# Kernel tuning notes

Hardware: AMD Instinct MI355X
Metric: run time of the kernel (lower is better)

## Reference

```python
import jax, jax.numpy as jnp
import numpy as np

B, S, D = 4, 2048, 1024


def setup_inputs() -> dict:
    key = jax.random.key(0)
    ks = jax.random.split(key, 9)
    scale = 1.0 / np.sqrt(D)
    x = jax.random.normal(ks[0], (B, S, D), dtype=jnp.float32)
    mask = jnp.tril(jnp.ones((S, S), dtype=jnp.int32))[None, :, :]  # causal, broadcast over batch
    Wq = jax.random.normal(ks[1], (D, D), dtype=jnp.float32) * scale
    bq = jax.random.normal(ks[2], (D,), dtype=jnp.float32) * 0.01
    Wk = jax.random.normal(ks[3], (D, D), dtype=jnp.float32) * scale
    bk = jax.random.normal(ks[4], (D,), dtype=jnp.float32) * 0.01
    Wv = jax.random.normal(ks[5], (D, D), dtype=jnp.float32) * scale
    bv = jax.random.normal(ks[6], (D,), dtype=jnp.float32) * 0.01
    Wo = jax.random.normal(ks[7], (D, D), dtype=jnp.float32) * scale
    bo = jax.random.normal(ks[8], (D,), dtype=jnp.float32) * 0.01
    return {"x": x, "mask": mask, "Wq": Wq, "bq": bq, "Wk": Wk, "bk": bk,
            "Wv": Wv, "bv": bv, "Wo": Wo, "bo": bo}


def reference(x, mask, Wq, bq, Wk, bk, Wv, bv, Wo, bo):
    # Linear projections (torch Linear: x @ W^T + b; here W stored as [in, out])
    Q = jnp.einsum('bsd,de->bse', x, Wq) + bq
    K = jnp.einsum('bsd,de->bse', x, Wk) + bk
    V = jnp.einsum('bsd,de->bse', x, Wv) + bv
    d_k = Q.shape[-1]
    scores = jnp.einsum('bqd,bkd->bqk', Q, K) / jnp.sqrt(jnp.float32(d_k))
    scores = jnp.where(mask == 0, jnp.float32(-jnp.inf), scores)
    attn_weights = jax.nn.softmax(scores, axis=-1)  # [B, S, S]
    attn_output = jnp.einsum('bqk,bkd->bqd', attn_weights, V)
    output = jnp.einsum('bsd,de->bse', attn_output, Wo) + bo
    return output, attn_weights
```

## Files before the change

kernel.cpp:

```cpp
#include <hip/hip_runtime.h>
#include <cstdint>
#include <cstddef>
#include <cmath>

typedef __bf16 bf16_t;
typedef bf16_t bf16x8 __attribute__((ext_vector_type(8)));
typedef bf16_t bf16x4 __attribute__((ext_vector_type(4)));
typedef float f32x4 __attribute__((ext_vector_type(4)));

constexpr int kB = 4;
constexpr int kS = 2048;
constexpr int kD = 1024;
constexpr int BM = 128, BN = 128, BK = 32;
constexpr int TILE_ELEMS = (BM + BN) * BK;

typedef __attribute__((address_space(1))) void as1void;
typedef __attribute__((address_space(3))) void as3void;

__device__ __forceinline__ void gload16(const void* g, void* l) {
  __builtin_amdgcn_global_load_lds((as1void*)g, (as3void*)l, 16, 0, 0);
}

__device__ __forceinline__ void wgbar() {
  asm volatile("" ::: "memory");
  __builtin_amdgcn_s_barrier();
  asm volatile("" ::: "memory");
}

__device__ __forceinline__ void gemm_mainloop(
    const bf16_t* __restrict__ A, int lda,
    const bf16_t* __restrict__ B, int ldb,
    int ksteps, bf16_t* lds, f32x4 acc[4][4]) {
  const int tid = threadIdx.x;
  const int w = tid >> 6, lane = tid & 63;
  const int srow = lane >> 2;
  const int scol = (lane & 3) << 3;
  const int wr = (w >> 1) << 6, wc = (w & 1) << 6;
  const int fr = lane & 15, kg = lane >> 4;

  const bf16_t* ga0 = A + (size_t)(w * 16 + srow) * lda + scol;
  const bf16_t* ga1 = A + (size_t)(64 + w * 16 + srow) * lda + scol;
  const bf16_t* gb0 = B + (size_t)(w * 16 + srow) * ldb + scol;
  const bf16_t* gb1 = B + (size_t)(64 + w * 16 + srow) * ldb + scol;
  const int oa0 = (w * 16) * BK;
  const int oa1 = (64 + w * 16) * BK;
  const int ob0 = BM * BK + (w * 16) * BK;
  const int ob1 = BM * BK + (64 + w * 16) * BK;

  gload16(ga0, lds + oa0);
  gload16(ga1, lds + oa1);
  gload16(gb0, lds + ob0);
  gload16(gb1, lds + ob1);
  ga0 += BK; ga1 += BK; gb0 += BK; gb1 += BK;
  __syncthreads();

  int cur = 0;
  for (int ks = 0; ks < ksteps; ++ks) {
    const int nxt = cur ^ 1;
    if (ks + 1 < ksteps) {
      bf16_t* nb = lds + nxt * TILE_ELEMS;
      gload16(ga0, nb + oa0);
      gload16(ga1, nb + oa1);
      gload16(gb0, nb + ob0);
      gload16(gb1, nb + ob1);
      ga0 += BK; ga1 += BK; gb0 += BK; gb1 += BK;
    }
    const bf16_t* cb = lds + cur * TILE_ELEMS;
    bf16x8 af[4], bfv[4];
#pragma unroll
    for (int m = 0; m < 4; ++m)
      af[m] = *(const bf16x8*)(cb + (wr + m * 16 + fr) * BK + kg * 8);
#pragma unroll
    for (int n = 0; n < 4; ++n)
      bfv[n] = *(const bf16x8*)(cb + BM * BK + (wc + n * 16 + fr) * BK + kg * 8);
#pragma unroll
    for (int m = 0; m < 4; ++m)
#pragma unroll
      for (int n = 0; n < 4; ++n)
        acc[m][n] = __builtin_amdgcn_mfma_f32_16x16x32_bf16(af[m], bfv[n],
                                                            acc[m][n], 0, 0, 0);
    __syncthreads();
    cur = nxt;
  }
}

__device__ __forceinline__ void gemm256_loop(
    const bf16_t* __restrict__ A, int lda,
    const bf16_t* __restrict__ B, int ldb,
    int nk, bf16_t* lds, f32x4 acc[8][4]) {
  const int tid = threadIdx.x;
  const int wid = tid >> 6, lane = tid & 63;
  const int wm = wid >> 2, wn = wid & 3;
  const int fr = lane & 15, kg = (lane >> 4) & 3;
  const int s_row = ((tid >> 7) << 4) | (tid & 15);
  const int s_col = ((tid >> 4) & 7) << 3;
  const bf16_t* pA = A + (size_t)s_row * lda + s_col;
  const bf16_t* pB = B + (size_t)s_row * ldb + s_col;
  const int ldst = wid << 9;

  auto stg = [&](int tt, int op, int h, int j) {
    const bf16_t* g = (op ? pB : pA) + (size_t)(h * 128 + j * 64) * (op ? ldb : lda)
                      + (size_t)tt * 64;
    bf16_t* d = lds + (((tt & 1) * 4 + op * 2 + h) * 8192) + j * 4096 + ldst;
    gload16(g, d);
  };

#pragma unroll
  for (int h = 0; h < 2; ++h)
#pragma unroll
    for (int j = 0; j < 2; ++j) { stg(0, 0, h, j); stg(0, 1, h, j); }
  stg(1, 1, 0, 0); stg(1, 1, 0, 1); stg(1, 1, 1, 0); stg(1, 1, 1, 1);
  stg(1, 0, 0, 0); stg(1, 0, 1, 0);
  asm volatile("s_waitcnt vmcnt(6)" ::: "memory");
  wgbar();

  const int arow = kg * 128 + fr * 8;
  for (int t = 0; t < nk; ++t) {
    const bf16_t* sb = lds + (t & 1) * 32768;
    const bf16_t* aslot = sb + wm * 8192;
    const bf16_t* bslot = sb + (2 + (wn >> 1)) * 8192 + (wn & 1) * 4096;
    bf16x8 bF[4][2];
#pragma unroll
    for (int q = 0; q < 4; ++q) {
      bf16x8 aF[2][2];
#pragma unroll
      for (int mi = 0; mi < 2; ++mi)
#pragma unroll
        for (int ks = 0; ks < 2; ++ks)
          aF[mi][ks] = *(const bf16x8*)(aslot + (2 * q + mi) * 1024 + ks * 512 + arow);
      if (q == 0) {
#pragma unroll
        for (int n = 0; n < 4; ++n)
#pragma unroll
          for (int ks = 0; ks < 2; ++ks)
            bF[n][ks] = *(const bf16x8*)(bslot + n * 1024 + ks * 512 + arow);
      }
      if (q == 0)      { if (t + 1 <= nk - 1) { stg(t + 1, 0, 0, 1); stg(t + 1, 0, 1, 1); } }
      else if (q == 1) { if (t + 2 <= nk - 1) { stg(t + 2, 1, 0, 0); stg(t + 2, 1, 0, 1); } }
      else if (q == 2) { if (t + 2 <= nk - 1) { stg(t + 2, 1, 1, 0); stg(t + 2, 1, 1, 1); } }
      else             { if (t + 2 <= nk - 1) { stg(t + 2, 0, 0, 0); stg(t + 2, 0, 1, 0); } }
      wgbar();
      __builtin_amdgcn_s_setprio(1);
#pragma unroll
      for (int mi = 0; mi < 2; ++mi)
#pragma unroll
        for (int n = 0; n < 4; ++n)
#pragma unroll
          for (int ks = 0; ks < 2; ++ks)
            acc[2 * q + mi][n] = __builtin_amdgcn_mfma_f32_16x16x32_bf16(
                aF[mi][ks], bF[n][ks], acc[2 * q + mi][n], 0, 0, 0);
      __builtin_amdgcn_s_setprio(0);
      asm volatile("s_waitcnt lgkmcnt(0)" ::: "memory");
      if (q == 3 && t < nk - 1) {
        if (t + 2 <= nk - 1) asm volatile("s_waitcnt vmcnt(6)" ::: "memory");
        else                 asm volatile("s_waitcnt vmcnt(0)" ::: "memory");
      }
      wgbar();
    }
  }
}


__global__ __launch_bounds__(512, 2)
void k_qk256(const bf16_t* __restrict__ A, const bf16_t* __restrict__ WT,
             const float* __restrict__ bq, const float* __restrict__ bk,
             bf16_t* __restrict__ Qb, bf16_t* __restrict__ Kb) {
  __shared__ bf16_t lds[65536];
  const int id = blockIdx.x;
  const int swz = (id & 7) * 32 + (id >> 3);
  const int mb = swz >> 3, nb = swz & 7;
  const int m0 = mb * 256, n0 = nb * 256;
  f32x4 acc[8][4] = {};
  gemm256_loop(A + (size_t)m0 * kD, kD, WT + (size_t)n0 * kD, kD,
               kD / 64, lds, acc);
  const int lane = threadIdx.x & 63, wid = threadIdx.x >> 6;
  const int wm = wid >> 2, wn = wid & 3, fr = lane & 15, kgr = lane >> 4;
  const int which = n0 >> 10;
  bf16_t* C = which == 0 ? Qb : Kb;
  const float* bias = which == 0 ? bq : bk;
#pragma unroll
  for (int n = 0; n < 4; ++n) {
    const int col = (n0 & 1023) + wn * 64 + n * 16 + fr;
    const float bvv = bias[col];
#pragma unroll
    for (int m = 0; m < 8; ++m)
#pragma unroll
      for (int i = 0; i < 4; ++i) {
        const int row = m0 + wm * 128 + m * 16 + kgr * 4 + i;
        C[(size_t)row * kD + col] = (bf16_t)(acc[m][n][i] + bvv);
      }
  }
}

__global__ __launch_bounds__(256)
void k_scores_v(const bf16_t* __restrict__ Q, const bf16_t* __restrict__ K,
                float* __restrict__ Sc,
                const bf16_t* __restrict__ X, const bf16_t* __restrict__ WvT,
                const float* __restrict__ bv, bf16_t* __restrict__ VT) {
  __shared__ bf16_t lds[2 * TILE_ELEMS];
  const int id = blockIdx.x;
  const int tid = threadIdx.x, w = tid >> 6, lane = tid & 63;
  const int wr = (w >> 1) << 6, wc = (w & 1) << 6, fr = lane & 15, kg = lane >> 4;
  if (id < 544) {
    const int b = id / 136, t = id % 136;
    int by = (int)((sqrtf(8.f * t + 1.f) - 1.f) * 0.5f);
    while ((by + 1) * (by + 2) / 2 <= t) ++by;
    while (by * (by + 1) / 2 > t) --by;
    const int bx = t - by * (by + 1) / 2;
    const int m0 = by * BM, n0 = bx * BN;
    f32x4 acc[4][4] = {};
    gemm_mainloop(Q + (size_t)b * kS * kD + (size_t)m0 * kD, kD,
                  K + (size_t)b * kS * kD + (size_t)n0 * kD, kD, kD / BK, lds, acc);
    float* Sb = Sc + (size_t)b * kS * kS;
#pragma unroll
    for (int m = 0; m < 4; ++m)
#pragma unroll
      for (int n = 0; n < 4; ++n)
#pragma unroll
        for (int i = 0; i < 4; ++i) {
          const int row = m0 + wr + m * 16 + kg * 4 + i;
          const int col = n0 + wc + n * 16 + fr;
          Sb[(size_t)row * kS + col] = acc[m][n][i] * 0.03125f;
        }
  } else {
    const int vid = id - 544;
    const int swz = (vid & 7) * 64 + (vid >> 3);
    const int m0 = (swz >> 3) * BM, n0 = (swz & 7) * BN;
    f32x4 acc[4][4] = {};
    gemm_mainloop(X + (size_t)m0 * kD, kD, WvT + (size_t)n0 * kD, kD,
                  kD / BK, lds, acc);
#pragma unroll
    for (int n = 0; n < 4; ++n) {
      const int col = n0 + wc + n * 16 + fr;
      const float bvv = bv[col];
#pragma unroll
      for (int m = 0; m < 4; ++m)
#pragma unroll
        for (int i = 0; i < 4; ++i) {
          const int row = m0 + wr + m * 16 + kg * 4 + i;
          const int b = row >> 11, s = row & (kS - 1);
          VT[((size_t)b * kD + col) * kS + s] = (bf16_t)(acc[m][n][i] + bvv);
        }
    }
  }
}

__global__ __launch_bounds__(256)
void k_softmax(float* __restrict__ P, bf16_t* __restrict__ Pb) {
  const int row = blockIdx.x;
  const int q = row & (kS - 1);
  float* p = P + (size_t)row * kS;
  bf16_t* pb = Pb + (size_t)row * kS;
  const int L = q + 1;
  __shared__ float buf[kS];
  __shared__ float red[8];
  const int tid = threadIdx.x;
  float4* b4 = (float4*)buf;
  const float4* p4 = (const float4*)p;
  if (tid * 4 < L) b4[tid] = p4[tid];
  if (1024 + tid * 4 < L) b4[tid + 256] = p4[tid + 256];
  __syncthreads();
  float mx = -1e30f;
  for (int k = tid; k < L; k += 256) mx = fmaxf(mx, buf[k]);
#pragma unroll
  for (int s2 = 32; s2 >= 1; s2 >>= 1) mx = fmaxf(mx, __shfl_xor(mx, s2));
  if ((tid & 63) == 0) red[tid >> 6] = mx;
  __syncthreads();
  mx = fmaxf(fmaxf(red[0], red[1]), fmaxf(red[2], red[3]));
  float sm = 0.f;
  for (int k = tid; k < L; k += 256) {
    const float e = __expf(buf[k] - mx);
    buf[k] = e;
    sm += e;
  }
#pragma unroll
  for (int s2 = 32; s2 >= 1; s2 >>= 1) sm += __shfl_xor(sm, s2);
  if ((tid & 63) == 0) red[4 + (tid >> 6)] = sm;
  __syncthreads();
  const float inv = 1.f / (red[4] + red[5] + red[6] + red[7]);
  for (int k = tid; k < L; k += 256) {
    const float v = buf[k] * inv;
    p[k] = v;
    pb[k] = (bf16_t)v;
  }
  for (int k = L + tid; k < kS; k += 256) p[k] = 0.f;
  const int bandEnd = (q & ~127) + 128;
  for (int k = L + tid; k < bandEnd; k += 256) pb[k] = (bf16_t)0.f;
}

__global__ __launch_bounds__(256)
void k_gemm_pv(const bf16_t* __restrict__ P, const bf16_t* __restrict__ VT,
               bf16_t* __restrict__ AO) {
  const int bx = blockIdx.x, b = blockIdx.z;
  const int by = (int)gridDim.y - 1 - (int)blockIdx.y;
  __shared__ bf16_t lds[2 * TILE_ELEMS];
  const int m0 = by * BM, n0 = bx * BN;
  const int ksteps = (m0 + BM) / BK;
  f32x4 acc[4][4] = {};
  gemm_mainloop(P + (size_t)b * kS * kS + (size_t)m0 * kS, kS,
                VT + (size_t)b * kD * kS + (size_t)n0 * kS, kS, ksteps, lds, acc);
  bf16_t* AOb = AO + (size_t)b * kS * kD;
  const int tid = threadIdx.x, w = tid >> 6, lane = tid & 63;
  const int wr = (w >> 1) << 6, wc = (w & 1) << 6, fr = lane & 15, kg = lane >> 4;
#pragma unroll
  for (int m = 0; m < 4; ++m)
#pragma unroll
    for (int n = 0; n < 4; ++n)
#pragma unroll
      for (int i = 0; i < 4; ++i) {
        const int row = m0 + wr + m * 16 + kg * 4 + i;
        const int col = n0 + wc + n * 16 + fr;
        AOb[(size_t)row * kD + col] = (bf16_t)acc[m][n][i];
      }
}

__global__ __launch_bounds__(256)
void k_gemm_out(const bf16_t* __restrict__ A, const bf16_t* __restrict__ Bw,
                const float* __restrict__ bias, float* __restrict__ C) {
  __shared__ bf16_t lds[2 * TILE_ELEMS];
  const int id = blockIdx.x;
  const int swz = (id & 7) * 64 + (id >> 3);
  const int m0 = (swz >> 3) * BM, n0 = (swz & 7) * BN;
  f32x4 acc[4][4] = {};
  gemm_mainloop(A + (size_t)m0 * kD, kD, Bw + (size_t)n0 * kD, kD, kD / BK, lds, acc);
  const int tid = threadIdx.x, w = tid >> 6, lane = tid & 63;
  const int wr = (w >> 1) << 6, wc = (w & 1) << 6, fr = lane & 15, kg = lane >> 4;
#pragma unroll
  for (int n = 0; n < 4; ++n) {
    const int col = n0 + wc + n * 16 + fr;
    const float bv = bias[col];
#pragma unroll
    for (int m = 0; m < 4; ++m)
#pragma unroll
      for (int i = 0; i < 4; ++i) {
        const int row = m0 + wr + m * 16 + kg * 4 + i;
        C[(size_t)row * kD + col] = acc[m][n][i] + bv;
      }
  }
}

__global__ __launch_bounds__(256)
void k_prep(const float* __restrict__ X, bf16_t* __restrict__ Y,
            const float* __restrict__ W0, const float* __restrict__ W1,
            const float* __restrict__ W2, const float* __restrict__ W3,
            bf16_t* __restrict__ T0, bf16_t* __restrict__ T1,
            bf16_t* __restrict__ T2, bf16_t* __restrict__ T3) {
  const int tx = threadIdx.x & 31, ty = threadIdx.x >> 5;
  if (blockIdx.z == 4) {
    const size_t n4 = (size_t)kB * kS * kD / 4;
    size_t i = ((size_t)blockIdx.y * 32 + blockIdx.x) * 256 + threadIdx.x;
    const size_t stride = (size_t)1024 * 256;
    const float4* X4 = (const float4*)X;
    bf16x4* Y4 = (bf16x4*)Y;
    for (; i < n4; i += stride) {
      const float4 v = X4[i];
      bf16x4 o = {(bf16_t)v.x, (bf16_t)v.y, (bf16_t)v.z, (bf16_t)v.w};
      Y4[i] = o;
    }
    return;
  }
  const float* W = blockIdx.z == 0 ? W0 : blockIdx.z == 1 ? W1 : blockIdx.z == 2 ? W2 : W3;
  bf16_t* T = blockIdx.z == 0 ? T0 : blockIdx.z == 1 ? T1 : blockIdx.z == 2 ? T2 : T3;
  __shared__ float t[32][33];
  const int x0 = blockIdx.x * 32, y0 = blockIdx.y * 32;
#pragma unroll
  for (int j = 0; j < 4; ++j)
    t[ty + 8 * j][tx] = W[(size_t)(y0 + ty + 8 * j) * kD + x0 + tx];
  __syncthreads();
#pragma unroll
  for (int j = 0; j < 4; ++j)
    T[(size_t)(x0 + ty + 8 * j) * kD + y0 + tx] = (bf16_t)t[tx][ty + 8 * j];
}

extern "C" void kernel_launch(void* const* d_in, const int* in_sizes, int n_in,
                              void* d_out, int out_size, void* d_ws, size_t ws_size,
                              hipStream_t stream) {
  (void)in_sizes; (void)n_in; (void)out_size; (void)ws_size;
  const float* x  = (const float*)d_in[0];
  const float* Wq = (const float*)d_in[2];
  const float* bq = (const float*)d_in[3];
  const float* Wk = (const float*)d_in[4];
  const float* bk = (const float*)d_in[5];
  const float* Wv = (const float*)d_in[6];
  const float* bv = (const float*)d_in[7];
  const float* Wo = (const float*)d_in[8];
  const float* bo = (const float*)d_in[9];

  float* out  = (float*)d_out;
  float* Pout = out + (size_t)kB * kS * kD;

  bf16_t* WqT = (bf16_t*)d_ws;
  bf16_t* WkT = WqT + (size_t)kD * kD;
  bf16_t* WvT = WkT + (size_t)kD * kD;
  bf16_t* WoT = WvT + (size_t)kD * kD;
  bf16_t* Qb  = WoT + (size_t)kD * kD;
  bf16_t* Kb  = Qb + (size_t)kB * kS * kD;
  bf16_t* VTb = Kb + (size_t)kB * kS * kD;
  bf16_t* Pb  = VTb + (size_t)kB * kS * kD;
  bf16_t* AOb = Pb + (size_t)kB * kS * kS;
  bf16_t* xb  = AOb + (size_t)kB * kS * kD;

  k_prep<<<dim3(32, 32, 5), 256, 0, stream>>>(x, xb, Wq, Wk, Wv, Wo,
                                              WqT, WkT, WvT, WoT);
  k_qk256<<<256, 512, 0, stream>>>(xb, WqT, bq, bk, Qb, Kb);
  k_scores_v<<<1056, 256, 0, stream>>>(Qb, Kb, Pout, xb, WvT, bv, VTb);
  k_softmax<<<kB * kS, 256, 0, stream>>>(Pout, Pb);
  k_gemm_pv<<<dim3(8, 16, kB), 256, 0, stream>>>(Pb, VTb, AOb);
  k_gemm_out<<<512, 256, 0, stream>>>(AOb, WoT, bo, out);
}
```

Measured before the change: 209.6 us.

## Move upper-triangle zeroing into scores kernel and register-resident softmax

The scores+V kernel gains 480 extra blocks that write zeros to the strictly upper-triangular 128x128 tiles of the fp32 attention-weight output. Block ids are interleaved so zeroing, QK^T and V-projection work mix across the grid. The softmax kernel keeps each row in registers as two float4 chunks instead of staging it through shared memory, and writes only up to the end of the diagonal band instead of zero-filling the whole row tail. The intent is to spread the large zero-fill writes across a GEMM-bound kernel and shorten the memory-bound softmax, at the cost of a larger grid and index remapping.

```diff
diff --git a/kernel.cpp b/kernel.cpp
--- a/kernel.cpp
+++ b/kernel.cpp
@@ -199,10 +199,11 @@
                 const float* __restrict__ bv, bf16_t* __restrict__ VT) {
   __shared__ bf16_t lds[2 * TILE_ELEMS];
   const int id = blockIdx.x;
+  const int wid0 = (id & 7) * 192 + (id >> 3);
   const int tid = threadIdx.x, w = tid >> 6, lane = tid & 63;
   const int wr = (w >> 1) << 6, wc = (w & 1) << 6, fr = lane & 15, kg = lane >> 4;
-  if (id < 544) {
-    const int b = id / 136, t = id % 136;
+  if (wid0 < 544) {
+    const int b = wid0 / 136, t = wid0 % 136;
     int by = (int)((sqrtf(8.f * t + 1.f) - 1.f) * 0.5f);
     while ((by + 1) * (by + 2) / 2 <= t) ++by;
     while (by * (by + 1) / 2 > t) --by;
@@ -222,10 +223,23 @@
           const int col = n0 + wc + n * 16 + fr;
           Sb[(size_t)row * kS + col] = acc[m][n][i] * 0.03125f;
         }
+  } else if (wid0 < 1024) {
+    const int zid = wid0 - 544;
+    const int b = zid / 120, u = zid % 120;
+    int r = (int)((1.f + sqrtf(8.f * u + 1.f)) * 0.5f);
+    while (r * (r - 1) / 2 > u) --r;
+    while ((r + 1) * r / 2 <= u) ++r;
+    const int c = u - r * (r - 1) / 2;
+    const int by = c, bx = r;
+    float* base = Sc + (size_t)b * kS * kS + (size_t)by * BM * kS + bx * BN;
+    const f32x4 z = {0.f, 0.f, 0.f, 0.f};
+    for (int i = tid; i < 128 * 32; i += 256) {
+      const int row = i >> 5, c4 = i & 31;
+      ((f32x4*)(base + (size_t)row * kS))[c4] = z;
+    }
   } else {
-    const int vid = id - 544;
-    const int swz = (vid & 7) * 64 + (vid >> 3);
-    const int m0 = (swz >> 3) * BM, n0 = (swz & 7) * BN;
+    const int vid = wid0 - 1024;
+    const int m0 = (vid >> 3) * BM, n0 = (vid & 7) * BN;
     f32x4 acc[4][4] = {};
     gemm_mainloop(X + (size_t)m0 * kD, kD, WvT + (size_t)n0 * kD, kD,
                   kD / BK, lds, acc);
@@ -249,43 +263,56 @@
 void k_softmax(float* __restrict__ P, bf16_t* __restrict__ Pb) {
   const int row = blockIdx.x;
   const int q = row & (kS - 1);
+  const int L = q + 1;
+  const int nch = (q >> 2) + 1;
+  const int nB = ((q & ~127) + 128) >> 2;
   float* p = P + (size_t)row * kS;
-  bf16_t* pb = Pb + (size_t)row * kS;
-  const int L = q + 1;
-  __shared__ float buf[kS];
+  f32x4* p4 = (f32x4*)p;
+  bf16x4* pb4 = (bf16x4*)(Pb + (size_t)row * kS);
+  const int tid = threadIdx.x;
+  const int c0 = tid, c1 = 256 + tid;
+  f32x4 v0 = {-1e30f, -1e30f, -1e30f, -1e30f}, v1 = v0;
+  if (c0 < nch) v0 = p4[c0];
+  if (c1 < nch) v1 = p4[c1];
+#pragma unroll
+  for (int j = 0; j < 4; ++j) {
+    if (4 * c0 + j >= L) v0[j] = -1e30f;
+    if (4 * c1 + j >= L) v1[j] = -1e30f;
+  }
+  float mx = -1e30f;
+#pragma unroll
+  for (int j = 0; j < 4; ++j) mx = fmaxf(mx, fmaxf(v0[j], v1[j]));
+#pragma unroll
+  for (int s2 = 32; s2 >= 1; s2 >>= 1) mx = fmaxf(mx, __shfl_xor(mx, s2));
   __shared__ float red[8];
-  const int tid = threadIdx.x;
-  float4* b4 = (float4*)buf;
-  const float4* p4 = (const float4*)p;
-  if (tid * 4 < L) b4[tid] = p4[tid];
-  if (1024 + tid * 4 < L) b4[tid + 256] = p4[tid + 256];
-  __syncthreads();
-  float mx = -1e30f;
-  for (int k = tid; k < L; k += 256) mx = fmaxf(mx, buf[k]);
-#pragma unroll
-  for (int s2 = 32; s2 >= 1; s2 >>= 1) mx = fmaxf(mx, __shfl_xor(mx, s2));
   if ((tid & 63) == 0) red[tid >> 6] = mx;
   __syncthreads();
   mx = fmaxf(fmaxf(red[0], red[1]), fmaxf(red[2], red[3]));
+  f32x4 e0, e1;
   float sm = 0.f;
-  for (int k = tid; k < L; k += 256) {
-    const float e = __expf(buf[k] - mx);
-    buf[k] = e;
-    sm += e;
+#pragma unroll
+  for (int j = 0; j < 4; ++j) {
+    e0[j] = (4 * c0 + j < L) ? __expf(v0[j] - mx) : 0.f;
+    e1[j] = (4 * c1 + j < L) ? __expf(v1[j] - mx) : 0.f;
+    sm += e0[j] + e1[j];
   }
 #pragma unroll
   for (int s2 = 32; s2 >= 1; s2 >>= 1) sm += __shfl_xor(sm, s2);
   if ((tid & 63) == 0) red[4 + (tid >> 6)] = sm;
   __syncthreads();
   const float inv = 1.f / (red[4] + red[5] + red[6] + red[7]);
-  for (int k = tid; k < L; k += 256) {
-    const float v = buf[k] * inv;
-    p[k] = v;
-    pb[k] = (bf16_t)v;
-  }
-  for (int k = L + tid; k < kS; k += 256) p[k] = 0.f;
-  const int bandEnd = (q & ~127) + 128;
-  for (int k = L + tid; k < bandEnd; k += 256) pb[k] = (bf16_t)0.f;
+  if (c0 < nB) {
+    f32x4 o; bf16x4 ob;
+#pragma unroll
+    for (int j = 0; j < 4; ++j) { o[j] = e0[j] * inv; ob[j] = (bf16_t)o[j]; }
+    p4[c0] = o; pb4[c0] = ob;
+  }
+  if (c1 < nB) {
+    f32x4 o; bf16x4 ob;
+#pragma unroll
+    for (int j = 0; j < 4; ++j) { o[j] = e1[j] * inv; ob[j] = (bf16_t)o[j]; }
+    p4[c1] = o; pb4[c1] = ob;
+  }
 }
 
 __global__ __launch_bounds__(256)
@@ -403,7 +430,7 @@
   k_prep<<<dim3(32, 32, 5), 256, 0, stream>>>(x, xb, Wq, Wk, Wv, Wo,
                                               WqT, WkT, WvT, WoT);
   k_qk256<<<256, 512, 0, stream>>>(xb, WqT, bq, bk, Qb, Kb);
-  k_scores_v<<<1056, 256, 0, stream>>>(Qb, Kb, Pout, xb, WvT, bv, VTb);
+  k_scores_v<<<1536, 256, 0, stream>>>(Qb, Kb, Pout, xb, WvT, bv, VTb);
   k_softmax<<<kB * kS, 256, 0, stream>>>(Pout, Pb);
   k_gemm_pv<<<dim3(8, 16, kB), 256, 0, stream>>>(Pb, VTb, AOb);
   k_gemm_out<<<512, 256, 0, stream>>>(AOb, WoT, bo, out);
```

Result: slower. 214.5 us (+2.3%).
